# Kernel optimization log

Measured on AMD Instinct MI355X. Metric: run time of the kernel, lower is better.

The kernel has to match this reference:

```python
import jax, jax.numpy as jnp
import numpy as np


def setup_inputs() -> dict:
    key = jax.random.key(0)
    kx, ks = jax.random.split(key)
    M, N, D = 8192, 8192, 512
    X = jax.random.normal(kx, (M, D), dtype=jnp.float32)
    svs = jax.random.normal(ks, (N, D), dtype=jnp.float32)
    # scale = 1/(2*sigma^2); a plausible fitted value for standard-normal data
    scale = jnp.asarray(0.01, dtype=jnp.float32)
    return {"X": X, "svs": svs, "scale": scale}


def reference(X, svs, scale):
    N, D = svs.shape
    x2 = jnp.sum(X * X, axis=-1, keepdims=True)          # [M, 1]
    s2 = jnp.sum(svs * svs, axis=-1)                      # [N]
    dist2 = x2 + s2[None, :] - 2.0 * (X @ svs.T)          # [M, N]
    dist2 = jnp.maximum(dist2, 0.0)
    log_p = (jax.scipy.special.logsumexp(-scale * dist2, axis=-1)
             - jnp.log(jnp.asarray(N, dtype=X.dtype))
             + (D / 2) * jnp.log(scale / jnp.pi))
    return log_p
```

## Files before the change

kernel.cpp:

```cpp
#include <hip/hip_runtime.h>
#include <hip/hip_bf16.h>
#include <hip/hip_fp8.h>
#include <math.h>

typedef __attribute__((ext_vector_type(4))) int   int4v;
typedef __attribute__((ext_vector_type(8))) int   int8v;
typedef __attribute__((ext_vector_type(4))) float f32x4;

#define BM 128
#define BN 128
#define BK 128

__global__ __launch_bounds__(256) void prep_kernel(
    const float* __restrict__ X, const float* __restrict__ S,
    unsigned char* __restrict__ Xq, unsigned char* __restrict__ Sq,
    float* __restrict__ x2, float* __restrict__ s2,
    float* __restrict__ rowsum, int M, int R, int Dv)
{
    const int gid  = blockIdx.x * 256 + threadIdx.x;
    const int nthr = gridDim.x * 256;

    for (int i = gid; i < M; i += nthr) rowsum[i] = 0.f;

    const int lane = threadIdx.x & 63;
    const int wid  = gid >> 6;
    const int nw   = nthr >> 6;

    for (int row = wid; row < R; row += nw) {
        const float* rp;
        unsigned char* op;
        float* sq;
        if (row < M) { rp = X + (size_t)row * Dv;       op = Xq + (size_t)row * Dv;       sq = x2 + row; }
        else         { rp = S + (size_t)(row - M) * Dv; op = Sq + (size_t)(row - M) * Dv; sq = s2 + (row - M); }

        float acc = 0.f;
        for (int k = lane * 8; k < Dv; k += 64 * 8) {
            float4 v0 = *(const float4*)(rp + k);
            float4 v1 = *(const float4*)(rp + k + 4);
            acc += v0.x * v0.x + v0.y * v0.y + v0.z * v0.z + v0.w * v0.w;
            acc += v1.x * v1.x + v1.y * v1.y + v1.z * v1.z + v1.w * v1.w;
            union { __hip_fp8_e4m3 h[8]; uint2 u; } pk;
            pk.h[0] = __hip_fp8_e4m3(v0.x);
            pk.h[1] = __hip_fp8_e4m3(v0.y);
            pk.h[2] = __hip_fp8_e4m3(v0.z);
            pk.h[3] = __hip_fp8_e4m3(v0.w);
            pk.h[4] = __hip_fp8_e4m3(v1.x);
            pk.h[5] = __hip_fp8_e4m3(v1.y);
            pk.h[6] = __hip_fp8_e4m3(v1.z);
            pk.h[7] = __hip_fp8_e4m3(v1.w);
            *(uint2*)(op + k) = pk.u;
        }
#pragma unroll
        for (int off = 1; off < 64; off <<= 1)
            acc += __shfl_xor(acc, off, 64);
        if (lane == 0) *sq = acc;
    }
}

template<int DVC>
__global__ __launch_bounds__(256, 3) void kde_gemm_kernel(
    const unsigned char* __restrict__ Xq,
    const unsigned char* __restrict__ Sq,
    const float* __restrict__ x2,
    const float* __restrict__ s2,
    const float* __restrict__ scale_p,
    float* __restrict__ rowsum,
    int M, int N, int Dv)
{
    const int D = DVC ? DVC : Dv;

    __shared__ char smem[32768];
    unsigned char* As = (unsigned char*)smem;
    unsigned char* Bs = (unsigned char*)(smem + 16384);

    const int tid  = threadIdx.x;
    const int wave = tid >> 6;
    const int lane = tid & 63;
    const int quad = lane >> 4;
    const int l16  = lane & 15;

    const int m0 = blockIdx.x * BM;
    const int n0 = blockIdx.y * BN;
    const int wm = (wave & 1) * 64;
    const int wn = (wave >> 1) * 64;

    const float sc = *scale_p;

    f32x4 acc[4][4] = {};

    const int srow0 = wave * 8 + (lane >> 3);
    const int cg    = (lane & 7) ^ (lane >> 3);
    const unsigned char* gA = Xq + (size_t)(m0 + srow0) * D + cg * 16;
    const unsigned char* gB = Sq + (size_t)(n0 + srow0) * D + cg * 16;

#pragma unroll
    for (int k0 = 0; k0 < D; k0 += BK) {
        __syncthreads();
#pragma unroll
        for (int rd = 0; rd < 4; ++rd)
            __builtin_amdgcn_global_load_lds(
                (const __attribute__((address_space(1))) void*)(gA + (size_t)rd * 32 * D + k0),
                (__attribute__((address_space(3))) void*)(smem + rd * 4096 + wave * 1024),
                16, 0, 0);
#pragma unroll
        for (int rd = 0; rd < 4; ++rd)
            __builtin_amdgcn_global_load_lds(
                (const __attribute__((address_space(1))) void*)(gB + (size_t)rd * 32 * D + k0),
                (__attribute__((address_space(3))) void*)(smem + 16384 + rd * 4096 + wave * 1024),
                16, 0, 0);
        __syncthreads();

        const int e = l16 & 7;
        int8v a_frag[4], b_frag[4];
#pragma unroll
        for (int mi = 0; mi < 4; ++mi) {
            const unsigned char* rowp = As + (wm + mi * 16 + l16) * 128;
            int4v lo = *(const int4v*)(rowp + ((2 * quad)     ^ e) * 16);
            int4v hi = *(const int4v*)(rowp + ((2 * quad + 1) ^ e) * 16);
            a_frag[mi] = (int8v){lo.x, lo.y, lo.z, lo.w, hi.x, hi.y, hi.z, hi.w};
        }
#pragma unroll
        for (int ni = 0; ni < 4; ++ni) {
            const unsigned char* rowp = Bs + (wn + ni * 16 + l16) * 128;
            int4v lo = *(const int4v*)(rowp + ((2 * quad)     ^ e) * 16);
            int4v hi = *(const int4v*)(rowp + ((2 * quad + 1) ^ e) * 16);
            b_frag[ni] = (int8v){lo.x, lo.y, lo.z, lo.w, hi.x, hi.y, hi.z, hi.w};
        }
#pragma unroll
        for (int mi = 0; mi < 4; ++mi)
#pragma unroll
            for (int ni = 0; ni < 4; ++ni)
                acc[mi][ni] = __builtin_amdgcn_mfma_scale_f32_16x16x128_f8f6f4(
                    a_frag[mi], b_frag[ni], acc[mi][ni],
                    0, 0,
                    0, 0x7F7F7F7F,
                    0, 0x7F7F7F7F);
    }

    __syncthreads();
    float* wred = (float*)smem + wave * (64 * 20);

    float s2v[4];
#pragma unroll
    for (int ni = 0; ni < 4; ++ni)
        s2v[ni] = s2[n0 + wn + ni * 16 + l16];

#pragma unroll
    for (int mi = 0; mi < 4; ++mi) {
#pragma unroll
        for (int r = 0; r < 4; ++r) {
            const int rowL = mi * 16 + quad * 4 + r;
            const float xv = x2[m0 + wm + rowL];
            float sum = 0.f;
#pragma unroll
            for (int ni = 0; ni < 4; ++ni) {
                float d2 = xv + s2v[ni] - 2.0f * acc[mi][ni][r];
                d2 = fmaxf(d2, 0.f);
                sum += __expf(-sc * d2);
            }
            wred[rowL * 20 + l16] = sum;
        }
    }
    __syncthreads();

    float4 p0 = *(float4*)(wred + lane * 20 + 0);
    float4 p1 = *(float4*)(wred + lane * 20 + 4);
    float4 p2 = *(float4*)(wred + lane * 20 + 8);
    float4 p3 = *(float4*)(wred + lane * 20 + 12);
    float s = (p0.x + p0.y + p0.z + p0.w) + (p1.x + p1.y + p1.z + p1.w)
            + (p2.x + p2.y + p2.z + p2.w) + (p3.x + p3.y + p3.z + p3.w);
    atomicAdd(&rowsum[m0 + wm + lane], s);
}

__global__ void finalize_kernel(const float* __restrict__ rowsum,
                                const float* __restrict__ scale_p,
                                float* __restrict__ out, int M, int N, int Dv) {
    const int m = blockIdx.x * 256 + threadIdx.x;
    if (m < M) {
        const float sc = *scale_p;
        const float cst = -logf((float)N) + 0.5f * (float)Dv * logf(sc / 3.14159265358979f);
        out[m] = logf(rowsum[m]) + cst;
    }
}

extern "C" void kernel_launch(void* const* d_in, const int* in_sizes, int n_in,
                              void* d_out, int out_size, void* d_ws, size_t ws_size,
                              hipStream_t stream) {
    const float* X       = (const float*)d_in[0];
    const float* S       = (const float*)d_in[1];
    const float* scale_p = (const float*)d_in[2];
    float* out = (float*)d_out;

    const int M  = out_size;
    const int Dv = in_sizes[0] / M;
    const int N  = in_sizes[1] / Dv;

    char* ws = (char*)d_ws;
    unsigned char* Xq = (unsigned char*)ws;
    unsigned char* Sq = (unsigned char*)(ws + (size_t)M * Dv);
    float* x2     = (float*)(ws + (size_t)M * Dv + (size_t)N * Dv);
    float* s2     = x2 + M;
    float* rowsum = s2 + N;

    prep_kernel<<<512, 256, 0, stream>>>(X, S, Xq, Sq, x2, s2, rowsum, M, M + N, Dv);

    dim3 grid(M / BM, N / BN);
    if (Dv == 512)
        kde_gemm_kernel<512><<<grid, 256, 0, stream>>>(Xq, Sq, x2, s2, scale_p, rowsum, M, N, Dv);
    else
        kde_gemm_kernel<0><<<grid, 256, 0, stream>>>(Xq, Sq, x2, s2, scale_p, rowsum, M, N, Dv);

    finalize_kernel<<<(M + 255) / 256, 256, 0, stream>>>(rowsum, scale_p, out, M, N, Dv);
}
```

Measured before the change: 121.4 us.

## Double-buffer LDS k-slabs in FP8 GEMM, packed fp8 convert, larger prep grid

The GEMM kernel now keeps two 32KB LDS buffers and prefetches slab t+2 while computing slab t. Partial vmcnt waits replace the full __syncthreads pair, so global-to-LDS loads can overlap the MFMAs. Occupancy drops from 3 to 2 blocks per CU because LDS use doubles. The prep kernel uses the packed cvt_pk_fp8_f32 builtin instead of per-element conversions and launches with a 4x larger grid.

```diff
diff --git a/kernel.cpp b/kernel.cpp
--- a/kernel.cpp
+++ b/kernel.cpp
@@ -10,6 +10,8 @@
 #define BM 128
 #define BN 128
 #define BK 128
+
+union frag_u { int8v v; int4v h[2]; };
 
 __global__ __launch_bounds__(256) void prep_kernel(
     const float* __restrict__ X, const float* __restrict__ S,
@@ -39,15 +41,12 @@
             float4 v1 = *(const float4*)(rp + k + 4);
             acc += v0.x * v0.x + v0.y * v0.y + v0.z * v0.z + v0.w * v0.w;
             acc += v1.x * v1.x + v1.y * v1.y + v1.z * v1.z + v1.w * v1.w;
-            union { __hip_fp8_e4m3 h[8]; uint2 u; } pk;
-            pk.h[0] = __hip_fp8_e4m3(v0.x);
-            pk.h[1] = __hip_fp8_e4m3(v0.y);
-            pk.h[2] = __hip_fp8_e4m3(v0.z);
-            pk.h[3] = __hip_fp8_e4m3(v0.w);
-            pk.h[4] = __hip_fp8_e4m3(v1.x);
-            pk.h[5] = __hip_fp8_e4m3(v1.y);
-            pk.h[6] = __hip_fp8_e4m3(v1.z);
-            pk.h[7] = __hip_fp8_e4m3(v1.w);
+            int lo = __builtin_amdgcn_cvt_pk_fp8_f32(v0.x, v0.y, 0, false);
+            lo     = __builtin_amdgcn_cvt_pk_fp8_f32(v0.z, v0.w, lo, true);
+            int hi = __builtin_amdgcn_cvt_pk_fp8_f32(v1.x, v1.y, 0, false);
+            hi     = __builtin_amdgcn_cvt_pk_fp8_f32(v1.z, v1.w, hi, true);
+            union { int i2[2]; uint2 u; } pk;
+            pk.i2[0] = lo; pk.i2[1] = hi;
             *(uint2*)(op + k) = pk.u;
         }
 #pragma unroll
@@ -58,7 +57,7 @@
 }
 
 template<int DVC>
-__global__ __launch_bounds__(256, 3) void kde_gemm_kernel(
+__global__ __launch_bounds__(256, 2) void kde_gemm_kernel(
     const unsigned char* __restrict__ Xq,
     const unsigned char* __restrict__ Sq,
     const float* __restrict__ x2,
@@ -67,11 +66,10 @@
     float* __restrict__ rowsum,
     int M, int N, int Dv)
 {
-    const int D = DVC ? DVC : Dv;
-
-    __shared__ char smem[32768];
-    unsigned char* As = (unsigned char*)smem;
-    unsigned char* Bs = (unsigned char*)(smem + 16384);
+    const int D  = DVC ? DVC : Dv;
+    const int NT = D / BK;
+
+    __shared__ char smem[65536];
 
     const int tid  = threadIdx.x;
     const int wave = tid >> 6;
@@ -93,45 +91,66 @@
     const unsigned char* gA = Xq + (size_t)(m0 + srow0) * D + cg * 16;
     const unsigned char* gB = Sq + (size_t)(n0 + srow0) * D + cg * 16;
 
-#pragma unroll
-    for (int k0 = 0; k0 < D; k0 += BK) {
-        __syncthreads();
-#pragma unroll
-        for (int rd = 0; rd < 4; ++rd)
+    auto stage = [&](int slab, int bufo) {
+        const size_t ko = (size_t)slab * BK;
+#pragma unroll
+        for (int rd = 0; rd < 4; ++rd) {
             __builtin_amdgcn_global_load_lds(
-                (const __attribute__((address_space(1))) void*)(gA + (size_t)rd * 32 * D + k0),
-                (__attribute__((address_space(3))) void*)(smem + rd * 4096 + wave * 1024),
+                (const __attribute__((address_space(1))) void*)(gA + (size_t)rd * 32 * D + ko),
+                (__attribute__((address_space(3))) void*)(smem + bufo + rd * 4096 + wave * 1024),
                 16, 0, 0);
-#pragma unroll
-        for (int rd = 0; rd < 4; ++rd)
             __builtin_amdgcn_global_load_lds(
-                (const __attribute__((address_space(1))) void*)(gB + (size_t)rd * 32 * D + k0),
-                (__attribute__((address_space(3))) void*)(smem + 16384 + rd * 4096 + wave * 1024),
+                (const __attribute__((address_space(1))) void*)(gB + (size_t)rd * 32 * D + ko),
+                (__attribute__((address_space(3))) void*)(smem + bufo + 16384 + rd * 4096 + wave * 1024),
                 16, 0, 0);
-        __syncthreads();
-
-        const int e = l16 & 7;
-        int8v a_frag[4], b_frag[4];
+        }
+    };
+
+    stage(0, 0);
+    if (NT > 1) stage(1, 32768);
+
+    const int e     = l16 & 7;
+    const int offLo = ((2 * quad)     ^ e) * 16;
+    const int offHi = ((2 * quad + 1) ^ e) * 16;
+    int aOff[4], bOff[4];
+#pragma unroll
+    for (int i = 0; i < 4; ++i) {
+        aOff[i] = (wm + i * 16 + l16) * 128;
+        bOff[i] = 16384 + (wn + i * 16 + l16) * 128;
+    }
+
+#pragma unroll
+    for (int t = 0; t < NT; ++t) {
+        if (t + 1 < NT) asm volatile("s_waitcnt vmcnt(8)" ::: "memory");
+        else            asm volatile("s_waitcnt vmcnt(0)" ::: "memory");
+        __builtin_amdgcn_s_barrier();
+
+        const int bufo = (t & 1) * 32768;
+        frag_u a_frag[4], b_frag[4];
 #pragma unroll
         for (int mi = 0; mi < 4; ++mi) {
-            const unsigned char* rowp = As + (wm + mi * 16 + l16) * 128;
-            int4v lo = *(const int4v*)(rowp + ((2 * quad)     ^ e) * 16);
-            int4v hi = *(const int4v*)(rowp + ((2 * quad + 1) ^ e) * 16);
-            a_frag[mi] = (int8v){lo.x, lo.y, lo.z, lo.w, hi.x, hi.y, hi.z, hi.w};
+            a_frag[mi].h[0] = *(const int4v*)(smem + bufo + aOff[mi] + offLo);
+            a_frag[mi].h[1] = *(const int4v*)(smem + bufo + aOff[mi] + offHi);
         }
 #pragma unroll
         for (int ni = 0; ni < 4; ++ni) {
-            const unsigned char* rowp = Bs + (wn + ni * 16 + l16) * 128;
-            int4v lo = *(const int4v*)(rowp + ((2 * quad)     ^ e) * 16);
-            int4v hi = *(const int4v*)(rowp + ((2 * quad + 1) ^ e) * 16);
-            b_frag[ni] = (int8v){lo.x, lo.y, lo.z, lo.w, hi.x, hi.y, hi.z, hi.w};
-        }
+            b_frag[ni].h[0] = *(const int4v*)(smem + bufo + bOff[ni] + offLo);
+            b_frag[ni].h[1] = *(const int4v*)(smem + bufo + bOff[ni] + offHi);
+        }
+
+        if (t + 2 < NT) {
+            asm volatile("s_waitcnt lgkmcnt(0)" ::: "memory");
+            __builtin_amdgcn_sched_barrier(0);
+            __builtin_amdgcn_s_barrier();
+            stage(t + 2, bufo);
+        }
+
 #pragma unroll
         for (int mi = 0; mi < 4; ++mi)
 #pragma unroll
             for (int ni = 0; ni < 4; ++ni)
                 acc[mi][ni] = __builtin_amdgcn_mfma_scale_f32_16x16x128_f8f6f4(
-                    a_frag[mi], b_frag[ni], acc[mi][ni],
+                    a_frag[mi].v, b_frag[ni].v, acc[mi][ni],
                     0, 0,
                     0, 0x7F7F7F7F,
                     0, 0x7F7F7F7F);
@@ -202,7 +221,7 @@
     float* s2     = x2 + M;
     float* rowsum = s2 + N;
 
-    prep_kernel<<<512, 256, 0, stream>>>(X, S, Xq, Sq, x2, s2, rowsum, M, M + N, Dv);
+    prep_kernel<<<2048, 256, 0, stream>>>(X, S, Xq, Sq, x2, s2, rowsum, M, M + N, Dv);
 
     dim3 grid(M / BM, N / BN);
     if (Dv == 512)
```

New measurement: 122.3 us. About the same (+0.8%).
